# Performance work log

Hardware: AMD Instinct MI355X
Metric: run time of the kernel (lower is better)

Reference implementation:

```python
import jax, jax.numpy as jnp
import numpy as np

B, T, D_MODEL, N_HEADS = 4, 2048, 1024, 16
D_K = D_MODEL // N_HEADS


def setup_inputs() -> dict:
    key = jax.random.key(0)
    kx, kq, kk, kv, ko = jax.random.split(key, 5)
    scale = 1.0 / np.sqrt(D_MODEL)  # ~ torch Linear init scale
    return {
        "x": jax.random.normal(kx, (B, T, D_MODEL), dtype=jnp.float32),
        "W_q": jax.random.uniform(kq, (D_MODEL, D_MODEL), jnp.float32, -scale, scale),
        "W_k": jax.random.uniform(kk, (D_MODEL, D_MODEL), jnp.float32, -scale, scale),
        "W_v": jax.random.uniform(kv, (D_MODEL, D_MODEL), jnp.float32, -scale, scale),
        "W_o": jax.random.uniform(ko, (D_MODEL, D_MODEL), jnp.float32, -scale, scale),
    }


def reference(x, W_q, W_k, W_v, W_o):
    b, t, _ = x.shape
    # nn.Linear(y) = y @ W.T ; split to (B, H, T, d_k)
    def split_heads(y):
        return y.reshape(b, t, N_HEADS, D_K).transpose(0, 2, 1, 3)

    Q = split_heads(x @ W_q.T)
    K = split_heads(x @ W_k.T)
    V = split_heads(x @ W_v.T)

    scores = jnp.einsum("bhqd,bhkd->bhqk", Q, K) / jnp.sqrt(jnp.float32(D_K))
    causal = jnp.triu(jnp.ones((t, t), dtype=bool), k=1)  # True = masked
    scores = jnp.where(causal, -jnp.inf, scores)
    weights = jax.nn.softmax(scores, axis=-1)
    out = jnp.einsum("bhqk,bhkd->bhqd", weights, V)
    out = out.transpose(0, 2, 1, 3).reshape(b, t, D_MODEL)
    return out @ W_o.T
```

## Files before the change

### kernel.cpp

```cpp
#include <hip/hip_runtime.h>

typedef __attribute__((ext_vector_type(8))) short s16x8;
typedef __attribute__((ext_vector_type(4))) float fx4;
typedef __attribute__((ext_vector_type(4))) int ix4;

#define B_SZ 4
#define T_SZ 2048
#define DM 1024
#define NH 16
#define DK 64
#define M_SZ (B_SZ * T_SZ)
#define NINF (-__builtin_inff())
#define QSCALE (0.125f * 1.44269504088896340736f)

__device__ __forceinline__ unsigned short f2bf(float f) {
    unsigned int u = __float_as_uint(f);
    unsigned int r = u + 0x7fffu + ((u >> 16) & 1u);
    return (unsigned short)(r >> 16);
}

__device__ __forceinline__ unsigned cvtpk(float lo, float hi) {
    unsigned r;
    asm("v_cvt_pk_bf16_f32 %0, %1, %2" : "=v"(r) : "v"(lo), "v"(hi));
    return r;
}

__device__ __forceinline__ void async16(const unsigned short* g, unsigned short* l) {
    __builtin_amdgcn_global_load_lds(
        (const __attribute__((address_space(1))) unsigned int*)g,
        (__attribute__((address_space(3))) unsigned int*)l, 16, 0, 0);
}

__global__ void cast_f32_bf16(const float* __restrict__ src, unsigned short* __restrict__ dst, int n) {
    int i = (blockIdx.x * blockDim.x + threadIdx.x) * 4;
    int stride = gridDim.x * blockDim.x * 4;
    for (; i + 3 < n; i += stride) {
        float4 v = *(const float4*)(src + i);
        ushort4 o;
        o.x = f2bf(v.x); o.y = f2bf(v.y); o.z = f2bf(v.z); o.w = f2bf(v.w);
        *(ushort4*)(dst + i) = o;
    }
}

__global__ void cast_w4(const float* __restrict__ s0, const float* __restrict__ s1,
                        const float* __restrict__ s2, const float* __restrict__ s3,
                        unsigned short* __restrict__ dst) {
    const float* s = (blockIdx.y == 0) ? s0 : (blockIdx.y == 1) ? s1 : (blockIdx.y == 2) ? s2 : s3;
    unsigned short* d = dst + (size_t)blockIdx.y * (DM * DM);
    int i = (blockIdx.x * blockDim.x + threadIdx.x) * 4;
    int stride = gridDim.x * blockDim.x * 4;
    for (; i + 3 < DM * DM; i += stride) {
        float4 v = *(const float4*)(s + i);
        ushort4 o;
        o.x = f2bf(v.x); o.y = f2bf(v.y); o.z = f2bf(v.z); o.w = f2bf(v.w);
        *(ushort4*)(d + i) = o;
    }
}

__global__ __launch_bounds__(256) void gemm_qkv(const unsigned short* __restrict__ A,
                                                const unsigned short* __restrict__ Wqkv,
                                                unsigned short* __restrict__ Qs,
                                                unsigned short* __restrict__ Kb,
                                                unsigned short* __restrict__ Vt) {
    __shared__ __align__(16) unsigned short smem[16896];

    const int t = threadIdx.x;
    const int lane = t & 63;
    const int w = t >> 6;
    const int wm = w >> 1, wn = w & 1;
    const int lrow = lane & 15, lk = lane >> 4;
    const int which = blockIdx.x >> 3;
    const int n0l = (blockIdx.x & 7) * 128;
    const int m0 = blockIdx.y * 128;
    const int K = DM;

    fx4 acc[4][4] = {};

    const int arow = t >> 2;
    const int acol = (t & 3) * 8;
    const unsigned short* Ag = A + (long)(m0 + arow) * K + acol;
    const unsigned short* Bg = Wqkv + (size_t)which * (DM * DM) + (long)(n0l + arow) * K + acol;
    const int lds0 = t * 8;
    const int nk = K / 32;

    async16(Ag, &smem[lds0]);
    async16(Ag + 64 * K, &smem[lds0 + 2048]);
    async16(Bg, &smem[8192 + lds0]);
    async16(Bg + 64 * K, &smem[8192 + lds0 + 2048]);

    for (int kt = 0; kt < nk; ++kt) {
        const int cur = kt & 1;
        if (kt + 1 < nk) {
            const int ko = (kt + 1) * 32;
            const int nb = (cur ^ 1) * 4096;
            async16(Ag + ko, &smem[nb + lds0]);
            async16(Ag + 64 * K + ko, &smem[nb + lds0 + 2048]);
            async16(Bg + ko, &smem[8192 + nb + lds0]);
            async16(Bg + 64 * K + ko, &smem[8192 + nb + lds0 + 2048]);
            asm volatile("s_waitcnt vmcnt(4)" ::: "memory");
        } else {
            asm volatile("s_waitcnt vmcnt(0)" ::: "memory");
        }
        __syncthreads();

        s16x8 af[4], bf[4];
#pragma unroll
        for (int i = 0; i < 4; ++i)
            af[i] = *(const s16x8*)&smem[cur * 4096 + (wm * 64 + i * 16 + lrow) * 32 + lk * 8];
#pragma unroll
        for (int i = 0; i < 4; ++i)
            bf[i] = *(const s16x8*)&smem[8192 + cur * 4096 + (wn * 64 + i * 16 + lrow) * 32 + lk * 8];
#pragma unroll
        for (int i = 0; i < 4; ++i)
#pragma unroll
            for (int j = 0; j < 4; ++j)
                acc[i][j] = __builtin_amdgcn_mfma_f32_16x16x32_bf16(af[i], bf[j], acc[i][j], 0, 0, 0);
        __syncthreads();
    }

    if (which < 2) {
        unsigned short* dst = (which == 0) ? Qs : Kb;
        const float sc = (which == 0) ? QSCALE : 1.f;
#pragma unroll
        for (int i = 0; i < 4; ++i)
#pragma unroll
            for (int j = 0; j < 4; ++j)
#pragma unroll
                for (int r = 0; r < 4; ++r) {
                    int row = m0 + wm * 64 + i * 16 + lk * 4 + r;
                    int col = n0l + wn * 64 + j * 16 + lrow;
                    dst[(long)row * DM + col] = f2bf(acc[i][j][r] * sc);
                }
    } else {
#pragma unroll
        for (int i = 0; i < 4; ++i)
#pragma unroll
            for (int j = 0; j < 4; ++j) {
                const int cl = wn * 64 + j * 16 + lrow;
                const int rl = wm * 64 + i * 16 + lk * 4;
                ushort4 pk;
                pk.x = f2bf(acc[i][j][0]); pk.y = f2bf(acc[i][j][1]);
                pk.z = f2bf(acc[i][j][2]); pk.w = f2bf(acc[i][j][3]);
                *(ushort4*)&smem[cl * 132 + rl] = pk;
            }
        __syncthreads();
        const int c = t >> 1, h2 = t & 1;
        unsigned short* vtp = Vt + (long)(n0l + c) * M_SZ + m0 + h2 * 64;
#pragma unroll
        for (int j = 0; j < 8; ++j) {
            union { struct { ushort4 a, b; } s; ix4 v; } u;
            u.s.a = *(const ushort4*)&smem[c * 132 + h2 * 64 + j * 8];
            u.s.b = *(const ushort4*)&smem[c * 132 + h2 * 64 + j * 8 + 4];
            *(ix4*)(vtp + j * 8) = u.v;
        }
    }
}

template<int OUT_BF16>
__global__ __launch_bounds__(256) void gemm_bt(const unsigned short* __restrict__ A,
                                               const unsigned short* __restrict__ Bw,
                                               void* __restrict__ Cout,
                                               int M, int N, int K, float scale) {
    __shared__ __align__(16) unsigned short As[2][128 * 32];
    __shared__ __align__(16) unsigned short Bs[2][128 * 32];

    const int t = threadIdx.x;
    const int lane = t & 63;
    const int w = t >> 6;
    const int wm = w >> 1, wn = w & 1;
    const int lrow = lane & 15, lk = lane >> 4;
    const int m0 = blockIdx.y * 128, n0 = blockIdx.x * 128;

    fx4 acc[4][4] = {};

    const int arow = t >> 2;
    const int acol = (t & 3) * 8;
    const unsigned short* Ag = A + (long)(m0 + arow) * K + acol;
    const unsigned short* Bg = Bw + (long)(n0 + arow) * K + acol;
    const int lds0 = t * 8;
    const int nk = K / 32;

    async16(Ag, &As[0][lds0]);
    async16(Ag + 64 * K, &As[0][lds0 + 64 * 32]);
    async16(Bg, &Bs[0][lds0]);
    async16(Bg + 64 * K, &Bs[0][lds0 + 64 * 32]);

    for (int kt = 0; kt < nk; ++kt) {
        const int cur = kt & 1;
        if (kt + 1 < nk) {
            const int ko = (kt + 1) * 32;
            async16(Ag + ko, &As[cur ^ 1][lds0]);
            async16(Ag + 64 * K + ko, &As[cur ^ 1][lds0 + 64 * 32]);
            async16(Bg + ko, &Bs[cur ^ 1][lds0]);
            async16(Bg + 64 * K + ko, &Bs[cur ^ 1][lds0 + 64 * 32]);
            asm volatile("s_waitcnt vmcnt(4)" ::: "memory");
        } else {
            asm volatile("s_waitcnt vmcnt(0)" ::: "memory");
        }
        __syncthreads();

        s16x8 af[4], bf[4];
#pragma unroll
        for (int i = 0; i < 4; ++i)
            af[i] = *(const s16x8*)&As[cur][(wm * 64 + i * 16 + lrow) * 32 + lk * 8];
#pragma unroll
        for (int i = 0; i < 4; ++i)
            bf[i] = *(const s16x8*)&Bs[cur][(wn * 64 + i * 16 + lrow) * 32 + lk * 8];
#pragma unroll
        for (int i = 0; i < 4; ++i)
#pragma unroll
            for (int j = 0; j < 4; ++j)
                acc[i][j] = __builtin_amdgcn_mfma_f32_16x16x32_bf16(af[i], bf[j], acc[i][j], 0, 0, 0);
        __syncthreads();
    }

#pragma unroll
    for (int i = 0; i < 4; ++i)
#pragma unroll
        for (int j = 0; j < 4; ++j)
#pragma unroll
            for (int r = 0; r < 4; ++r) {
                int row = m0 + wm * 64 + i * 16 + lk * 4 + r;
                int col = n0 + wn * 64 + j * 16 + lrow;
                float v = acc[i][j][r] * scale;
                if (OUT_BF16)
                    ((unsigned short*)Cout)[(long)row * N + col] = f2bf(v);
                else
                    ((float*)Cout)[(long)row * N + col] = v;
            }
}

__global__ __launch_bounds__(256, 4) void attn_kernel(const unsigned short* __restrict__ Q,
                                                      const unsigned short* __restrict__ Kb,
                                                      const unsigned short* __restrict__ Vt,
                                                      unsigned short* __restrict__ O) {
    __shared__ __align__(16) unsigned short Ks[2][64 * 64];
    __shared__ __align__(16) unsigned short Vs[2][64 * 64];
    __shared__ __align__(16) unsigned short Pl[4][16 * 72];

    const int t = threadIdx.x;
    const int lane = t & 63, w = t >> 6;
    const int lrow = lane & 15, lk = lane >> 4;
    const int hb = blockIdx.x;
    const int h = hb & 15, b = hb >> 4;
    const int qb = 15 - blockIdx.y;
    const int row0 = b * T_SZ;
    const int q0w = qb * 128 + w * 32;

    s16x8 qf[2][2];
#pragma unroll
    for (int hh = 0; hh < 2; ++hh) {
        const unsigned short* qp = Q + (long)(row0 + q0w + hh * 16 + lrow) * DM + h * DK + lk * 8;
        qf[hh][0] = *(const s16x8*)qp;
        qf[hh][1] = *(const s16x8*)(qp + 32);
    }

    fx4 acc[2][4] = {};
    float mrun[2] = {NINF, NINF}, lsum[2] = {0.f, 0.f};

    const int srow = t >> 3;
    const int chk = (t & 7) ^ (srow & 7);
    const unsigned short* Kg = Kb + (long)(row0 + srow) * DM + h * DK + chk * 8;
    const unsigned short* Vg = Vt + (long)(h * DK + srow) * M_SZ + row0 + chk * 8;
    unsigned short* Kl = &Ks[0][t * 8];
    unsigned short* Vl = &Vs[0][t * 8];

    const int nt = 2 * qb + 2;

    async16(Kg, Kl);
    async16(Kg + 32 * DM, Kl + 2048);
    async16(Vg, Vl);
    async16(Vg + 32 * (long)M_SZ, Vl + 2048);
    asm volatile("s_waitcnt vmcnt(0)" ::: "memory");
    __syncthreads();

    for (int kt = 0; kt < nt; ++kt) {
        const int cur = kt & 1;
        const bool pre = (kt + 1 < nt);
        if (pre) {
            const long koff = (long)(kt + 1) * 64 * DM;
            const int voff = (kt + 1) * 64;
            async16(Kg + koff, Kl + (cur ^ 1) * 4096);
            async16(Kg + koff + 32 * DM, Kl + (cur ^ 1) * 4096 + 2048);
            async16(Vg + voff, Vl + (cur ^ 1) * 4096);
            async16(Vg + voff + 32 * (long)M_SZ, Vl + (cur ^ 1) * 4096 + 2048);
        }
        const int kv0 = kt * 64;
        if (kv0 <= q0w + 31) {
            const char* ksb = (const char*)&Ks[cur][0];
            float p[2][4][4];
            float pm0 = NINF, pm1 = NINF;
#pragma unroll
            for (int sub = 0; sub < 4; ++sub) {
                const int kv0s = kv0 + sub * 16;
                if (kv0s <= q0w + 31) {
                    const int rb = (sub * 16 + lrow) << 7;
                    const int sw = (lrow & 7) << 4;
                    const s16x8 kf0 = *(const s16x8*)(ksb + (rb + ((lk * 16) ^ sw)));
                    const s16x8 kf1 = *(const s16x8*)(ksb + (rb + ((64 + lk * 16) ^ sw)));
                    fx4 s1 = {};
                    s1 = __builtin_amdgcn_mfma_f32_16x16x32_bf16(kf0, qf[1][0], s1, 0, 0, 0);
                    s1 = __builtin_amdgcn_mfma_f32_16x16x32_bf16(kf1, qf[1][1], s1, 0, 0, 0);
                    if (kv0s + 15 > q0w + 16) {
#pragma unroll
                        for (int r = 0; r < 4; ++r)
                            if (kv0s + lk * 4 + r > q0w + 16 + lrow) s1[r] = NINF;
                    }
#pragma unroll
                    for (int r = 0; r < 4; ++r) { p[1][sub][r] = s1[r]; pm1 = fmaxf(pm1, s1[r]); }
                    if (kv0s <= q0w + 15) {
                        fx4 s0 = {};
                        s0 = __builtin_amdgcn_mfma_f32_16x16x32_bf16(kf0, qf[0][0], s0, 0, 0, 0);
                        s0 = __builtin_amdgcn_mfma_f32_16x16x32_bf16(kf1, qf[0][1], s0, 0, 0, 0);
                        if (kv0s + 15 > q0w) {
#pragma unroll
                            for (int r = 0; r < 4; ++r)
                                if (kv0s + lk * 4 + r > q0w + lrow) s0[r] = NINF;
                        }
#pragma unroll
                        for (int r = 0; r < 4; ++r) { p[0][sub][r] = s0[r]; pm0 = fmaxf(pm0, s0[r]); }
                    } else {
#pragma unroll
                        for (int r = 0; r < 4; ++r) p[0][sub][r] = NINF;
                    }
                } else {
#pragma unroll
                    for (int r = 0; r < 4; ++r) { p[0][sub][r] = NINF; p[1][sub][r] = NINF; }
                }
            }
            float pmv[2] = {pm0, pm1};
#pragma unroll
            for (int hh = 0; hh < 2; ++hh) {
                float pm = pmv[hh];
                pm = fmaxf(pm, __shfl_xor(pm, 16));
                pm = fmaxf(pm, __shfl_xor(pm, 32));
                if (__any(pm > mrun[hh] + 8.f)) {
                    const float mnew = fmaxf(mrun[hh], pm);
                    const float sc = exp2f(mrun[hh] - mnew);
                    mrun[hh] = mnew;
                    lsum[hh] *= sc;
#pragma unroll
                    for (int r = 0; r < 4; ++r) {
                        const float scr = __shfl(sc, lk * 4 + r);
                        acc[hh][0][r] *= scr; acc[hh][1][r] *= scr;
                        acc[hh][2][r] *= scr; acc[hh][3][r] *= scr;
                    }
                }
                float ps = 0.f;
#pragma unroll
                for (int sub = 0; sub < 4; ++sub)
#pragma unroll
                    for (int r = 0; r < 4; ++r) {
                        const float pv = exp2f(p[hh][sub][r] - mrun[hh]);
                        p[hh][sub][r] = pv;
                        ps += pv;
                    }
                ps += __shfl_xor(ps, 16);
                ps += __shfl_xor(ps, 32);
                lsum[hh] += ps;
            }
            s16x8 pf[2][2];
#pragma unroll
            for (int hh = 0; hh < 2; ++hh) {
#pragma unroll
                for (int sub = 0; sub < 4; ++sub) {
                    uint2 pw;
                    pw.x = cvtpk(p[hh][sub][0], p[hh][sub][1]);
                    pw.y = cvtpk(p[hh][sub][2], p[hh][sub][3]);
                    *(uint2*)&Pl[w][lrow * 72 + sub * 16 + lk * 4] = pw;
                }
                pf[hh][0] = *(const s16x8*)&Pl[w][lrow * 72 + lk * 8];
                pf[hh][1] = *(const s16x8*)&Pl[w][lrow * 72 + 32 + lk * 8];
            }
#pragma unroll
            for (int s = 0; s < 2; ++s) {
                if (kv0 + s * 32 <= q0w + 31) {
                    const bool h0a = (kv0 + s * 32 <= q0w + 15);
#pragma unroll
                    for (int nf = 0; nf < 4; ++nf) {
                        const int d = nf * 16 + lrow;
                        const s16x8 vf = *(const s16x8*)&Vs[cur][d * 64 + (((s * 4 + lk) ^ (lrow & 7)) << 3)];
                        if (h0a)
                            acc[0][nf] = __builtin_amdgcn_mfma_f32_16x16x32_bf16(pf[0][s], vf, acc[0][nf], 0, 0, 0);
                        acc[1][nf] = __builtin_amdgcn_mfma_f32_16x16x32_bf16(pf[1][s], vf, acc[1][nf], 0, 0, 0);
                    }
                }
            }
        }
        asm volatile("s_waitcnt vmcnt(0)" ::: "memory");
        __syncthreads();
    }

#pragma unroll
    for (int hh = 0; hh < 2; ++hh) {
        float linv[4];
#pragma unroll
        for (int r = 0; r < 4; ++r) linv[r] = 1.f / __shfl(lsum[hh], lk * 4 + r);
        unsigned short* op = O + (long)(row0 + q0w + hh * 16) * DM + h * DK;
#pragma unroll
        for (int nf = 0; nf < 4; ++nf)
#pragma unroll
            for (int r = 0; r < 4; ++r)
                op[(long)(lk * 4 + r) * DM + nf * 16 + lrow] = f2bf(acc[hh][nf][r] * linv[r]);
    }
}

extern "C" void kernel_launch(void* const* d_in, const int* in_sizes, int n_in,
                              void* d_out, int out_size, void* d_ws, size_t ws_size,
                              hipStream_t stream) {
    const float* x  = (const float*)d_in[0];
    const float* Wq = (const float*)d_in[1];
    const float* Wk = (const float*)d_in[2];
    const float* Wv = (const float*)d_in[3];
    const float* Wo = (const float*)d_in[4];
    float* out = (float*)d_out;

    unsigned short* wsu = (unsigned short*)d_ws;
    unsigned short* xb  = wsu;
    unsigned short* wqb = xb + 8388608;
    unsigned short* wob = wqb + 3 * 1048576;
    unsigned short* Qs  = wob + 1048576;
    unsigned short* Ob  = Qs + 8388608;

    unsigned short* Kb = (unsigned short*)d_out;
    unsigned short* Vt = Kb + 8388608;

    cast_f32_bf16<<<2048, 256, 0, stream>>>(x, xb, M_SZ * DM);
    cast_w4<<<dim3(256, 4), 256, 0, stream>>>(Wq, Wk, Wv, Wo, wqb);

    gemm_qkv<<<dim3(24, M_SZ / 128), 256, 0, stream>>>(xb, wqb, Qs, Kb, Vt);

    dim3 agrid(64, 16);
    attn_kernel<<<agrid, 256, 0, stream>>>(Qs, Kb, Vt, Ob);

    dim3 ggrid(DM / 128, M_SZ / 128);
    gemm_bt<0><<<ggrid, 256, 0, stream>>>(Ob, wob, out, M_SZ, DM, DM, 1.f);
}
```

Baseline: 208.4 us.

## Widen QKV GEMM tile to 128x256 with 512 threads, BK=64 and swizzled LDS

```diff
diff --git a/kernel.cpp b/kernel.cpp
--- a/kernel.cpp
+++ b/kernel.cpp
@@ -57,91 +57,101 @@
     }
 }
 
-__global__ __launch_bounds__(256) void gemm_qkv(const unsigned short* __restrict__ A,
-                                                const unsigned short* __restrict__ Wqkv,
-                                                unsigned short* __restrict__ Qs,
-                                                unsigned short* __restrict__ Kb,
-                                                unsigned short* __restrict__ Vt) {
-    __shared__ __align__(16) unsigned short smem[16896];
+__global__ __launch_bounds__(512, 2) void gemm_qkv256(const unsigned short* __restrict__ A,
+                                                      const unsigned short* __restrict__ W,
+                                                      unsigned short* __restrict__ Qs,
+                                                      unsigned short* __restrict__ Kb,
+                                                      unsigned short* __restrict__ Vt) {
+    __shared__ __align__(16) unsigned short S[49152];
 
     const int t = threadIdx.x;
-    const int lane = t & 63;
-    const int w = t >> 6;
-    const int wm = w >> 1, wn = w & 1;
+    const int lane = t & 63, w = t >> 6;
+    const int wm = w >> 2, wn = w & 3;
     const int lrow = lane & 15, lk = lane >> 4;
-    const int which = blockIdx.x >> 3;
-    const int n0l = (blockIdx.x & 7) * 128;
+    const int bx = blockIdx.x;
     const int m0 = blockIdx.y * 128;
     const int K = DM;
+    const int NKT = K / 64;
 
     fx4 acc[4][4] = {};
 
-    const int arow = t >> 2;
-    const int acol = (t & 3) * 8;
-    const unsigned short* Ag = A + (long)(m0 + arow) * K + acol;
-    const unsigned short* Bg = Wqkv + (size_t)which * (DM * DM) + (long)(n0l + arow) * K + acol;
-    const int lds0 = t * 8;
-    const int nk = K / 32;
-
-    async16(Ag, &smem[lds0]);
-    async16(Ag + 64 * K, &smem[lds0 + 2048]);
-    async16(Bg, &smem[8192 + lds0]);
-    async16(Bg + 64 * K, &smem[8192 + lds0 + 2048]);
-
-    for (int kt = 0; kt < nk; ++kt) {
+    const int srow = t >> 3;
+    const int cs = (t & 7) ^ (srow & 7);
+    const unsigned short* Ag = A + (long)(m0 + srow) * K + cs * 8;
+    const unsigned short* Bg = W + (long)(bx * 256 + srow) * K + cs * 8;
+
+    async16(Ag,           &S[t * 8]);
+    async16(Ag + 64 * K,  &S[4096 + t * 8]);
+    async16(Bg,           &S[16384 + t * 8]);
+    async16(Bg + 64 * K,  &S[16384 + 4096 + t * 8]);
+    async16(Bg + 128 * K, &S[16384 + 8192 + t * 8]);
+    async16(Bg + 192 * K, &S[16384 + 12288 + t * 8]);
+    asm volatile("s_waitcnt vmcnt(0)" ::: "memory");
+    __syncthreads();
+
+    for (int kt = 0; kt < NKT; ++kt) {
         const int cur = kt & 1;
-        if (kt + 1 < nk) {
-            const int ko = (kt + 1) * 32;
-            const int nb = (cur ^ 1) * 4096;
-            async16(Ag + ko, &smem[nb + lds0]);
-            async16(Ag + 64 * K + ko, &smem[nb + lds0 + 2048]);
-            async16(Bg + ko, &smem[8192 + nb + lds0]);
-            async16(Bg + 64 * K + ko, &smem[8192 + nb + lds0 + 2048]);
-            asm volatile("s_waitcnt vmcnt(4)" ::: "memory");
-        } else {
-            asm volatile("s_waitcnt vmcnt(0)" ::: "memory");
-        }
+        if (kt + 1 < NKT) {
+            const int ko = (kt + 1) * 64;
+            const int nbA = (cur ^ 1) * 8192;
+            const int nbB = 16384 + (cur ^ 1) * 16384;
+            async16(Ag + ko,           &S[nbA + t * 8]);
+            async16(Ag + 64 * K + ko,  &S[nbA + 4096 + t * 8]);
+            async16(Bg + ko,           &S[nbB + t * 8]);
+            async16(Bg + 64 * K + ko,  &S[nbB + 4096 + t * 8]);
+            async16(Bg + 128 * K + ko, &S[nbB + 8192 + t * 8]);
+            async16(Bg + 192 * K + ko, &S[nbB + 12288 + t * 8]);
+        }
+        const unsigned short* Ab = &S[cur * 8192];
+        const unsigned short* Bb = &S[16384 + cur * 16384];
+#pragma unroll
+        for (int kk = 0; kk < 2; ++kk) {
+            const int sw = ((kk * 4 + lk) ^ (lrow & 7)) * 8;
+            s16x8 af[4], bf[4];
+#pragma unroll
+            for (int mf = 0; mf < 4; ++mf)
+                af[mf] = *(const s16x8*)&Ab[(wm * 64 + mf * 16 + lrow) * 64 + sw];
+#pragma unroll
+            for (int nf = 0; nf < 4; ++nf)
+                bf[nf] = *(const s16x8*)&Bb[(wn * 64 + nf * 16 + lrow) * 64 + sw];
+            __builtin_amdgcn_s_setprio(1);
+#pragma unroll
+            for (int mf = 0; mf < 4; ++mf)
+#pragma unroll
+                for (int nf = 0; nf < 4; ++nf)
+                    acc[mf][nf] = __builtin_amdgcn_mfma_f32_16x16x32_bf16(af[mf], bf[nf], acc[mf][nf], 0, 0, 0);
+            __builtin_amdgcn_s_setprio(0);
+        }
+        asm volatile("s_waitcnt vmcnt(0)" ::: "memory");
         __syncthreads();
-
-        s16x8 af[4], bf[4];
-#pragma unroll
-        for (int i = 0; i < 4; ++i)
-            af[i] = *(const s16x8*)&smem[cur * 4096 + (wm * 64 + i * 16 + lrow) * 32 + lk * 8];
-#pragma unroll
-        for (int i = 0; i < 4; ++i)
-            bf[i] = *(const s16x8*)&smem[8192 + cur * 4096 + (wn * 64 + i * 16 + lrow) * 32 + lk * 8];
-#pragma unroll
-        for (int i = 0; i < 4; ++i)
-#pragma unroll
-            for (int j = 0; j < 4; ++j)
-                acc[i][j] = __builtin_amdgcn_mfma_f32_16x16x32_bf16(af[i], bf[j], acc[i][j], 0, 0, 0);
-        __syncthreads();
-    }
-
+    }
+
+    const int which = bx >> 2;
+    const int n0l = (bx & 3) * 256;
     if (which < 2) {
-        unsigned short* dst = (which == 0) ? Qs : Kb;
-        const float sc = (which == 0) ? QSCALE : 1.f;
-#pragma unroll
-        for (int i = 0; i < 4; ++i)
-#pragma unroll
-            for (int j = 0; j < 4; ++j)
+        unsigned short* dst = which ? Kb : Qs;
+        const float sc = which ? 1.f : QSCALE;
+#pragma unroll
+        for (int mf = 0; mf < 4; ++mf)
+#pragma unroll
+            for (int nf = 0; nf < 4; ++nf)
 #pragma unroll
                 for (int r = 0; r < 4; ++r) {
-                    int row = m0 + wm * 64 + i * 16 + lk * 4 + r;
-                    int col = n0l + wn * 64 + j * 16 + lrow;
-                    dst[(long)row * DM + col] = f2bf(acc[i][j][r] * sc);
+                    int row = m0 + wm * 64 + mf * 16 + lk * 4 + r;
+                    int col = n0l + wn * 64 + nf * 16 + lrow;
+                    dst[(long)row * DM + col] = f2bf(acc[mf][nf][r] * sc);
                 }
     } else {
 #pragma unroll
-        for (int i = 0; i < 4; ++i)
-#pragma unroll
-            for (int j = 0; j < 4; ++j) {
-                const int cl = wn * 64 + j * 16 + lrow;
-                const int rl = wm * 64 + i * 16 + lk * 4;
+        for (int mf = 0; mf < 4; ++mf)
+#pragma unroll
+            for (int nf = 0; nf < 4; ++nf) {
+                const int cl = wn * 64 + nf * 16 + lrow;
+                const int rl = wm * 64 + mf * 16 + lk * 4;
                 ushort4 pk;
-                pk.x = f2bf(acc[i][j][0]); pk.y = f2bf(acc[i][j][1]);
-                pk.z = f2bf(acc[i][j][2]); pk.w = f2bf(acc[i][j][3]);
-                *(ushort4*)&smem[cl * 132 + rl] = pk;
+                pk.x = f2bf(acc[mf][nf][0]); pk.y = f2bf(acc[mf][nf][1]);
+                pk.z = f2bf(acc[mf][nf][2]); pk.w = f2bf(acc[mf][nf][3]);
+                *(ushort4*)&S[cl * 132 + rl] = pk;
             }
         __syncthreads();
         const int c = t >> 1, h2 = t & 1;
@@ -149,8 +159,8 @@
 #pragma unroll
         for (int j = 0; j < 8; ++j) {
             union { struct { ushort4 a, b; } s; ix4 v; } u;
-            u.s.a = *(const ushort4*)&smem[c * 132 + h2 * 64 + j * 8];
-            u.s.b = *(const ushort4*)&smem[c * 132 + h2 * 64 + j * 8 + 4];
+            u.s.a = *(const ushort4*)&S[c * 132 + h2 * 64 + j * 8];
+            u.s.b = *(const ushort4*)&S[c * 132 + h2 * 64 + j * 8 + 4];
             *(ix4*)(vtp + j * 8) = u.v;
         }
     }
@@ -428,7 +438,7 @@
     cast_f32_bf16<<<2048, 256, 0, stream>>>(x, xb, M_SZ * DM);
     cast_w4<<<dim3(256, 4), 256, 0, stream>>>(Wq, Wk, Wv, Wo, wqb);
 
-    gemm_qkv<<<dim3(24, M_SZ / 128), 256, 0, stream>>>(xb, wqb, Qs, Kb, Vt);
+    gemm_qkv256<<<dim3(12, M_SZ / 128), 512, 0, stream>>>(xb, wqb, Qs, Kb, Vt);
 
     dim3 agrid(64, 16);
     attn_kernel<<<agrid, 256, 0, stream>>>(Qs, Kb, Vt, Ob);
```

Result: faster. 198.9 us (-4.5%).
